# Optimization experiments

Hardware: AMD Instinct MI355X
Metric: run time of the kernel (lower is better)

Reference implementation:

```python
import jax, jax.numpy as jnp
import numpy as np

GYRO_COV = 0.00016968 ** 2
ACC_COV = 0.002 ** 2
GRAVITY = 9.81007


def _skew(v):
    # v: (..., 3) -> (..., 3, 3)
    x, y, z = v[..., 0], v[..., 1], v[..., 2]
    O = jnp.zeros_like(x)
    return jnp.stack([
        jnp.stack([O, -z, y], -1),
        jnp.stack([z, O, -x], -1),
        jnp.stack([-y, x, O], -1)], -2)


def _exp_and_jr(w):
    """SO3 Exp map (rotation matrix) and right Jacobian of w = omega*dt. w: (B,3)."""
    t2 = jnp.sum(w * w, axis=-1)[..., None, None]          # (B,1,1)
    small = t2 < 1e-8
    t2s = jnp.where(small, 1.0, t2)                        # safe denominators
    t = jnp.sqrt(t2s)
    A = jnp.where(small, 1.0 - t2 / 6.0, jnp.sin(t) / t)           # sin(t)/t
    Bc = jnp.where(small, 0.5 - t2 / 24.0, (1.0 - jnp.cos(t)) / t2s)  # (1-cos)/t^2
    C = jnp.where(small, 1.0 / 6.0 - t2 / 120.0, (t - jnp.sin(t)) / (t2s * t))  # (t-sin)/t^3
    K = _skew(w)
    K2 = K @ K
    I = jnp.eye(3, dtype=w.dtype)
    R = I + A * K + Bc * K2
    Jr = I - Bc * K + C * K2
    return R, Jr


def _preintegrate(dt, gyro, acc, init_pos, init_rot, init_vel):
    B, F = dt.shape[0], dt.shape[1]
    dtype = dt.dtype
    I3 = jnp.eye(3, dtype=dtype)

    def step(carry, xs):
        Dr, Dv, Dp, cov, t = carry
        dtk, wk, ak = xs                      # (B,1), (B,3), (B,3)
        dR, Jr = _exp_and_jr(wk * dtk)        # (B,3,3) each
        Ra = jnp.einsum('bij,bj->bi', Dr, ak) # Delta_R_ik @ a_k
        Dp_n = Dp + Dv * dtk + 0.5 * Ra * dtk ** 2
        Dv_n = Dv + Ra * dtk
        Dr_n = Dr @ dR
        # --- 9x9 covariance propagation ---
        dt_ = dtk[..., None]                  # (B,1,1)
        Ha = (Dr @ _skew(ak))                 # Delta_R_ik @ skew(a_k)
        Ib = jnp.broadcast_to(I3, Ha.shape)
        Z = jnp.zeros_like(Ha)
        A = jnp.concatenate([
            jnp.concatenate([jnp.swapaxes(dR, -1, -2), Z, Z], -1),
            jnp.concatenate([-Ha * dt_, Ib, Z], -1),
            jnp.concatenate([-0.5 * Ha * dt_ ** 2, Ib * dt_, Ib], -1)], -2)  # (B,9,9)
        Bg = Jr * dt_                                                        # (B,3,3)
        Ba = jnp.concatenate([Dr * dt_, 0.5 * Dr * dt_ ** 2], -2)           # (B,6,3)
        Ng = GYRO_COV * (Bg @ jnp.swapaxes(Bg, -1, -2))
        Na = ACC_COV * (Ba @ jnp.swapaxes(Ba, -1, -2))
        N = jnp.zeros_like(cov).at[:, :3, :3].set(Ng).at[:, 3:, 3:].set(Na)
        cov_n = A @ cov @ jnp.swapaxes(A, -1, -2) + N
        t_n = t + dtk
        return (Dr_n, Dv_n, Dp_n, cov_n, t_n), (Dr_n, Dv_n, Dp_n, t_n)

    carry0 = (jnp.broadcast_to(I3, (B, 3, 3)),
              jnp.zeros((B, 3), dtype),
              jnp.zeros((B, 3), dtype),
              jnp.zeros((B, 9, 9), dtype),
              jnp.zeros((B, 1), dtype))
    xs = (jnp.moveaxis(dt, 1, 0), jnp.moveaxis(gyro, 1, 0), jnp.moveaxis(acc, 1, 0))
    (Dr, Dv, Dp, cov, t), (Drs, Dvs, Dps, ts) = jax.lax.scan(step, carry0, xs)
    Drs = jnp.moveaxis(Drs, 0, 1)   # (B,F,3,3)
    Dvs = jnp.moveaxis(Dvs, 0, 1)   # (B,F,3)
    Dps = jnp.moveaxis(Dps, 0, 1)   # (B,F,3)
    ts = jnp.moveaxis(ts, 0, 1)     # (B,F,1)
    grav = jnp.array([0.0, 0.0, GRAVITY], dtype=dtype)
    rot = jnp.einsum('ij,bfjk->bfik', init_rot, Drs)                       # R_j = R_i * dR_ij
    vel = init_vel + jnp.einsum('ij,bfj->bfi', init_rot, Dvs) - grav * ts
    pos = (init_pos + init_vel * ts
           + jnp.einsum('ij,bfj->bfi', init_rot, Dps) - 0.5 * grav * ts ** 2)
    return rot, vel, pos, cov


def setup_inputs() -> dict:
    key = jax.random.key(0)
    k1, k2, k3 = jax.random.split(key, 3)
    B, F = 512, 2048
    dt = 0.004 * jax.random.uniform(k1, (B, F, 1), dtype=jnp.float32) + 0.001  # ~200-1000Hz
    gyro = 0.5 * jax.random.normal(k2, (B, F, 3), dtype=jnp.float32)
    acc = 2.0 * jax.random.normal(k3, (B, F, 3), dtype=jnp.float32)
    return {"dt": dt, "gyro": gyro, "acc": acc,
            "init_pos": jnp.zeros(3, jnp.float32),
            "init_rot": jnp.eye(3, dtype=jnp.float32),
            "init_vel": jnp.zeros(3, jnp.float32)}


def reference(dt, gyro, acc, init_pos, init_rot, init_vel):
    return _preintegrate(dt, gyro, acc, init_pos, init_rot, init_vel)
```

## Files before the change

kernel.cpp:

```cpp
#include <hip/hip_runtime.h>
#include <cstddef>

#define FCNT 2048
#define SEG 512
#define LSTEP 4

#define GRAV 9.81007f
#define GYRO_COV (0.00016968f * 0.00016968f)
#define ACC_COV (0.002f * 0.002f)

__device__ __forceinline__ void exp_coefs(float t2, float& A, float& Bc, float& Cc) {
  A  = 1.f     + t2 * (-1.f/6.f   + t2 * (1.f/120.f  + t2 * (-1.f/5040.f)));
  Bc = 0.5f    + t2 * (-1.f/24.f  + t2 * (1.f/720.f  + t2 * (-1.f/40320.f)));
  Cc = 1.f/6.f + t2 * (-1.f/120.f + t2 * (1.f/5040.f + t2 * (-1.f/362880.f)));
  if (t2 > 0.004f) {
    float t = sqrtf(t2);
    float sn = __sinf(t), cs = __cosf(t);
    A  = sn / t;
    Bc = (1.f - cs) / t2;
    Cc = (t - sn) / (t2 * t);
  }
}

__device__ __forceinline__ void make_dR(float w0, float w1, float w2, float t2,
                                        float A, float Bc, float* dR) {
  float w01 = w0*w1, w02 = w0*w2, w12 = w1*w2;
  dR[0] = 1.f + Bc*(w0*w0 - t2); dR[1] = Bc*w01 - A*w2;         dR[2] = Bc*w02 + A*w1;
  dR[3] = Bc*w01 + A*w2;         dR[4] = 1.f + Bc*(w1*w1 - t2); dR[5] = Bc*w12 - A*w0;
  dR[6] = Bc*w02 - A*w1;         dR[7] = Bc*w12 + A*w0;         dR[8] = 1.f + Bc*(w2*w2 - t2);
}

__device__ __forceinline__ void mm3(const float* a, const float* b, float* c) {
#pragma unroll
  for (int i = 0; i < 3; ++i) {
    float a0 = a[i*3+0], a1 = a[i*3+1], a2 = a[i*3+2];
    c[i*3+0] = a0*b[0] + a1*b[3] + a2*b[6];
    c[i*3+1] = a0*b[1] + a1*b[4] + a2*b[7];
    c[i*3+2] = a0*b[2] + a1*b[5] + a2*b[8];
  }
}

__device__ __forceinline__ void conjT(const float* R, const float* Mp, float* M) {
  float tmp[9];
#pragma unroll
  for (int i = 0; i < 3; ++i)
#pragma unroll
    for (int j = 0; j < 3; ++j)
      tmp[i*3+j] = R[0+i]*Mp[0+j] + R[3+i]*Mp[3+j] + R[6+i]*Mp[6+j];
  mm3(tmp, R, M);
}

__device__ __forceinline__ void compose16(const float* pa, const float* stv, float* o) {
  float nR[9];
  mm3(pa, stv, nR);
  float nv0 = pa[9]  + pa[0]*stv[9] + pa[1]*stv[10] + pa[2]*stv[11];
  float nv1 = pa[10] + pa[3]*stv[9] + pa[4]*stv[10] + pa[5]*stv[11];
  float nv2 = pa[11] + pa[6]*stv[9] + pa[7]*stv[10] + pa[8]*stv[11];
  float qt = stv[15];
  float np0 = pa[12] + pa[9]*qt  + pa[0]*stv[12] + pa[1]*stv[13] + pa[2]*stv[14];
  float np1 = pa[13] + pa[10]*qt + pa[3]*stv[12] + pa[4]*stv[13] + pa[5]*stv[14];
  float np2 = pa[14] + pa[11]*qt + pa[6]*stv[12] + pa[7]*stv[13] + pa[8]*stv[14];
  float nt = pa[15] + qt;
#pragma unroll
  for (int i = 0; i < 9; ++i) o[i] = nR[i];
  o[9]=nv0; o[10]=nv1; o[11]=nv2;
  o[12]=np0; o[13]=np1; o[14]=np2;
  o[15]=nt;
}

__device__ __forceinline__ void set_identity16(float* o) {
  o[0]=1;o[1]=0;o[2]=0; o[3]=0;o[4]=1;o[5]=0; o[6]=0;o[7]=0;o[8]=1;
#pragma unroll
  for (int i = 9; i < 16; ++i) o[i] = 0.f;
}

__device__ __forceinline__ void load_seg(const float* __restrict__ dtp,
                                         const float* __restrict__ gyp,
                                         const float* __restrict__ acp,
                                         size_t base, float* dl, float* gl, float* al) {
  const float4 x0 = *reinterpret_cast<const float4*>(dtp + base);
  dl[0]=x0.x; dl[1]=x0.y; dl[2]=x0.z; dl[3]=x0.w;
  const float4* qg = reinterpret_cast<const float4*>(gyp + base*3);
  const float4* qa = reinterpret_cast<const float4*>(acp + base*3);
#pragma unroll
  for (int i = 0; i < 3; ++i) {
    float4 xg = qg[i];
    gl[i*4+0]=xg.x; gl[i*4+1]=xg.y; gl[i*4+2]=xg.z; gl[i*4+3]=xg.w;
    float4 xa = qa[i];
    al[i*4+0]=xa.x; al[i*4+1]=xa.y; al[i*4+2]=xa.z; al[i*4+3]=xa.w;
  }
}

__device__ __forceinline__ void integrate_seg(const float* dl, const float* gl,
                                              const float* al, float* st) {
  set_identity16(st);
#pragma unroll
  for (int j = 0; j < LSTEP; ++j) {
    float dd = dl[j];
    float w0 = gl[j*3+0]*dd, w1 = gl[j*3+1]*dd, w2 = gl[j*3+2]*dd;
    float t2 = w0*w0 + w1*w1 + w2*w2;
    float A, Bc, Cc;
    exp_coefs(t2, A, Bc, Cc);
    (void)Cc;
    float dR[9];
    make_dR(w0, w1, w2, t2, A, Bc, dR);
    float a0 = al[j*3+0], a1 = al[j*3+1], a2 = al[j*3+2];
    float Ra0 = st[0]*a0 + st[1]*a1 + st[2]*a2;
    float Ra1 = st[3]*a0 + st[4]*a1 + st[5]*a2;
    float Ra2 = st[6]*a0 + st[7]*a1 + st[8]*a2;
    float hh = 0.5f*dd*dd;
    st[12] += st[9]*dd  + hh*Ra0;
    st[13] += st[10]*dd + hh*Ra1;
    st[14] += st[11]*dd + hh*Ra2;
    st[9] += Ra0*dd; st[10] += Ra1*dd; st[11] += Ra2*dd;
    float Rn[9];
    mm3(st, dR, Rn);
#pragma unroll
    for (int i = 0; i < 9; ++i) st[i] = Rn[i];
    st[15] += dd;
  }
}

__global__ __launch_bounds__(SEG, 2)
void imu_fused(const float* __restrict__ dtp, const float* __restrict__ gyp,
               const float* __restrict__ acp, const float* __restrict__ ip0,
               const float* __restrict__ iR0, const float* __restrict__ iv0,
               float* __restrict__ out, int B)
{
  __shared__ float rstage[FCNT*9];
  __shared__ float wtot[16*8];
  __shared__ float rbuf[8][48];
  __shared__ float tsum[48];

  const int s = threadIdx.x;
  const int lane = s & 63;
  const int wid = s >> 6;
  const int b = blockIdx.x;
  const size_t base = (size_t)b*FCNT + (size_t)s*LSTEP;
  const size_t NBF = (size_t)B*FCNT;
  float* orot = out;
  float* ovel = out + NBF*9;
  float* opos = out + NBF*12;
  float* ocov = out + NBF*15;

  float st[16];
  {
    float dl[LSTEP], gl[LSTEP*3], al[LSTEP*3];
    load_seg(dtp, gyp, acp, base, dl, gl, al);
    integrate_seg(dl, gl, al, st);
  }

#pragma unroll
  for (int off = 1; off < 64; off <<= 1) {
    float pa[16];
#pragma unroll
    for (int i = 0; i < 16; ++i) pa[i] = __shfl_up(st[i], off);
    if (lane >= off) compose16(pa, st, st);
  }
  if (lane == 63) {
#pragma unroll
    for (int i = 0; i < 16; ++i) wtot[i*8 + wid] = st[i];
  }
  __syncthreads();
  if (s < 8) {
    float t[16];
#pragma unroll
    for (int i = 0; i < 16; ++i) t[i] = wtot[i*8 + s];
#pragma unroll
    for (int off = 1; off < 8; off <<= 1) {
      float pa[16];
#pragma unroll
      for (int i = 0; i < 16; ++i) pa[i] = __shfl_up(t[i], off);
      if (s >= off) compose16(pa, t, t);
    }
#pragma unroll
    for (int i = 0; i < 16; ++i) wtot[i*8 + s] = t[i];
  }
  __syncthreads();

  float TF[16];
#pragma unroll
  for (int i = 0; i < 16; ++i) TF[i] = wtot[i*8 + 7];

  float cr[16];
  {
    float lex[16];
#pragma unroll
    for (int i = 0; i < 16; ++i) lex[i] = __shfl_up(st[i], 1);
    if (lane == 0) set_identity16(lex);
    if (wid == 0) {
#pragma unroll
      for (int i = 0; i < 16; ++i) cr[i] = lex[i];
    } else {
      float wx[16];
#pragma unroll
      for (int i = 0; i < 16; ++i) wx[i] = wtot[i*8 + wid - 1];
      compose16(wx, lex, cr);
    }
  }

  float R0g[9];
#pragma unroll
  for (int i = 0; i < 9; ++i) R0g[i] = iR0[i];
  const float p0x = ip0[0], p0y = ip0[1], p0z = ip0[2];
  const float v0x = iv0[0], v0y = iv0[1], v0z = iv0[2];

  const float Tt = TF[15];
  const float Tvp0 = R0g[0]*TF[9] + R0g[1]*TF[10] + R0g[2]*TF[11];
  const float Tvp1 = R0g[3]*TF[9] + R0g[4]*TF[10] + R0g[5]*TF[11];
  const float Tvp2 = R0g[6]*TF[9] + R0g[7]*TF[10] + R0g[8]*TF[11];
  const float Tpp0 = R0g[0]*TF[12] + R0g[1]*TF[13] + R0g[2]*TF[14];
  const float Tpp1 = R0g[3]*TF[12] + R0g[4]*TF[13] + R0g[5]*TF[14];
  const float Tpp2 = R0g[6]*TF[12] + R0g[7]*TF[13] + R0g[8]*TF[14];

  float tR[9];
  mm3(R0g, cr, tR);
  float tv0 = R0g[0]*cr[9] + R0g[1]*cr[10] + R0g[2]*cr[11];
  float tv1 = R0g[3]*cr[9] + R0g[4]*cr[10] + R0g[5]*cr[11];
  float tv2 = R0g[6]*cr[9] + R0g[7]*cr[10] + R0g[8]*cr[11];
  float tp0 = R0g[0]*cr[12] + R0g[1]*cr[13] + R0g[2]*cr[14];
  float tp1 = R0g[3]*cr[12] + R0g[4]*cr[13] + R0g[5]*cr[14];
  float tp2 = R0g[6]*cr[12] + R0g[7]*cr[13] + R0g[8]*cr[14];
  float ctt = cr[15];

  float dl[LSTEP], gl[LSTEP*3], al[LSTEP*3];
  load_seg(dtp, gyp, acp, base, dl, gl, al);

  float aS0=0,aS1=0,aS2=0,aS3=0,aS4=0,aS5=0;
  float aU0=0,aU1=0,aU2=0,aU3=0,aU4=0,aU5=0,aU6=0,aU7=0,aU8=0;
  float aV0=0,aV1=0,aV2=0,aV3=0,aV4=0,aV5=0,aV6=0,aV7=0,aV8=0;
  float b220=0,b221=0,b222=0,b223=0,b224=0,b225=0;
  float b230=0,b231=0,b232=0,b233=0,b234=0,b235=0,b236=0,b237=0,b238=0;
  float b330=0,b331=0,b332=0,b333=0,b334=0,b335=0;
  float sa=0.f, sb=0.f, sc=0.f;
  float vloc[LSTEP*3], ploc[LSTEP*3];

#pragma unroll
  for (int j = 0; j < LSTEP; ++j) {
    const float dd = dl[j];
    const float w0 = gl[j*3+0]*dd, w1 = gl[j*3+1]*dd, w2 = gl[j*3+2]*dd;
    const float t2 = w0*w0 + w1*w1 + w2*w2;
    float A, Bc, Cc;
    exp_coefs(t2, A, Bc, Cc);
    float dR[9];
    make_dR(w0, w1, w2, t2, A, Bc, dR);
    const float a0 = al[j*3+0], a1 = al[j*3+1], a2 = al[j*3+2];
    const float Ra0 = tR[0]*a0 + tR[1]*a1 + tR[2]*a2;
    const float Ra1 = tR[3]*a0 + tR[4]*a1 + tR[5]*a2;
    const float Ra2 = tR[6]*a0 + tR[7]*a1 + tR[8]*a2;
    const float hh = 0.5f*dd*dd;
    tp0 += tv0*dd + hh*Ra0;
    tp1 += tv1*dd + hh*Ra1;
    tp2 += tv2*dd + hh*Ra2;
    tv0 += Ra0*dd; tv1 += Ra1*dd; tv2 += Ra2*dd;
    float Rn[9];
    mm3(tR, dR, Rn);
#pragma unroll
    for (int i = 0; i < 9; ++i) {
      tR[i] = Rn[i];
      rstage[((size_t)s*LSTEP + j)*9 + i] = Rn[i];
    }
    ctt += dd;
    vloc[j*3+0] = v0x + tv0;
    vloc[j*3+1] = v0y + tv1;
    vloc[j*3+2] = v0z + tv2 - GRAV*ctt;
    ploc[j*3+0] = p0x + v0x*ctt + tp0;
    ploc[j*3+1] = p0y + v0y*ctt + tp1;
    ploc[j*3+2] = p0z + v0z*ctt + tp2 - 0.5f*GRAV*ctt*ctt;

    const float sg  = GYRO_COV*dd*dd;
    const float eps = 2.f*Cc - Bc*Bc - Cc*Cc*t2;
    const float alpha = sg*(1.f - eps*t2);
    const float beta  = sg*eps;
    const float u0 = tR[0]*w0 + tR[1]*w1 + tR[2]*w2;
    const float u1 = tR[3]*w0 + tR[4]*w1 + tR[5]*w2;
    const float u2 = tR[6]*w0 + tR[7]*w1 + tR[8]*w2;
    const float z = Tt - ctt;
    const float wv0 = Tvp0 - tv0, wv1 = Tvp1 - tv1, wv2 = Tvp2 - tv2;
    const float wp0 = Tpp0 - tp0 - z*tv0;
    const float wp1 = Tpp1 - tp1 - z*tv1;
    const float wp2 = Tpp2 - tp2 - z*tv2;
    const float c0 = wv1*u2 - wv2*u1;
    const float c1 = wv2*u0 - wv0*u2;
    const float c2 = wv0*u1 - wv1*u0;
    const float d0 = wp1*u2 - wp2*u1;
    const float d1 = wp2*u0 - wp0*u2;
    const float d2 = wp0*u1 - wp1*u0;
    const float bu0 = beta*u0, bu1 = beta*u1, bu2 = beta*u2;
    const float bc0 = beta*c0, bc1 = beta*c1, bc2 = beta*c2;
    const float bd0 = beta*d0, bd1 = beta*d1, bd2 = beta*d2;
    const float av0 = alpha*wv0, av1 = alpha*wv1, av2 = alpha*wv2;
    const float ap0 = alpha*wp0, ap1 = alpha*wp1, ap2 = alpha*wp2;
    const float nv2_ = wv0*wv0 + wv1*wv1 + wv2*wv2;
    const float np2_ = wp0*wp0 + wp1*wp1 + wp2*wp2;
    const float dvp  = wv0*wp0 + wv1*wp1 + wv2*wp2;
    aS0 += alpha + bu0*u0; aS1 += bu0*u1; aS2 += bu0*u2;
    aS3 += alpha + bu1*u1; aS4 += bu1*u2; aS5 += alpha + bu2*u2;
    aU0 += -bu0*c0;        aU1 += -av2 - bu0*c1;  aU2 +=  av1 - bu0*c2;
    aU3 +=  av2 - bu1*c0;  aU4 += -bu1*c1;        aU5 += -av0 - bu1*c2;
    aU6 += -av1 - bu2*c0;  aU7 +=  av0 - bu2*c1;  aU8 += -bu2*c2;
    aV0 += -bu0*d0;        aV1 += -ap2 - bu0*d1;  aV2 +=  ap1 - bu0*d2;
    aV3 +=  ap2 - bu1*d0;  aV4 += -bu1*d1;        aV5 += -ap0 - bu1*d2;
    aV6 += -ap1 - bu2*d0;  aV7 +=  ap0 - bu2*d1;  aV8 += -bu2*d2;
    b220 += av0*wv0 - alpha*nv2_ - bc0*c0;
    b221 += av0*wv1 - bc0*c1;
    b222 += av0*wv2 - bc0*c2;
    b223 += av1*wv1 - alpha*nv2_ - bc1*c1;
    b224 += av1*wv2 - bc1*c2;
    b225 += av2*wv2 - alpha*nv2_ - bc2*c2;
    b230 += ap0*wv0 - alpha*dvp - bc0*d0;
    b231 += ap0*wv1 - bc0*d1;
    b232 += ap0*wv2 - bc0*d2;
    b233 += ap1*wv0 - bc1*d0;
    b234 += ap1*wv1 - alpha*dvp - bc1*d1;
    b235 += ap1*wv2 - bc1*d2;
    b236 += ap2*wv0 - bc2*d0;
    b237 += ap2*wv1 - bc2*d1;
    b238 += ap2*wv2 - alpha*dvp - bc2*d2;
    b330 += ap0*wp0 - alpha*np2_ - bd0*d0;
    b331 += ap0*wp1 - bd0*d1;
    b332 += ap0*wp2 - bd0*d2;
    b333 += ap1*wp1 - alpha*np2_ - bd1*d1;
    b334 += ap1*wp2 - bd1*d2;
    b335 += ap2*wp2 - alpha*np2_ - bd2*d2;
    const float dsq = dd*dd;
    const float aa = ACC_COV*dsq;
    const float bbq = 0.5f*ACC_COV*dsq*dd;
    sa += aa;
    sb += aa*z + bbq;
    sc += z*(aa*z + 2.f*bbq) + 0.25f*ACC_COV*dsq*dsq;
  }
  __syncthreads();

  {
    const float4* sm4 = reinterpret_cast<const float4*>(rstage);
    float4* g4 = reinterpret_cast<float4*>(orot + (size_t)b * FCNT * 9);
#pragma unroll
    for (int k = 0; k < 9; ++k)
      g4[k*SEG + s] = sm4[k*SEG + s];
  }
  {
    float4* vq = reinterpret_cast<float4*>(ovel + base*3);
#pragma unroll
    for (int k = 0; k < LSTEP*3/4; ++k)
      vq[k] = make_float4(vloc[k*4+0], vloc[k*4+1], vloc[k*4+2], vloc[k*4+3]);
    float4* pq = reinterpret_cast<float4*>(opos + base*3);
#pragma unroll
    for (int k = 0; k < LSTEP*3/4; ++k)
      pq[k] = make_float4(ploc[k*4+0], ploc[k*4+1], ploc[k*4+2], ploc[k*4+3]);
  }

  {
    float red[48] = {aS0,aS1,aS2,aS3,aS4,aS5,
                     aU0,aU1,aU2,aU3,aU4,aU5,aU6,aU7,aU8,
                     aV0,aV1,aV2,aV3,aV4,aV5,aV6,aV7,aV8,
                     b220,b221,b222,b223,b224,b225,
                     b230,b231,b232,b233,b234,b235,b236,b237,b238,
                     b330,b331,b332,b333,b334,b335,
                     sa,sb,sc};
#pragma unroll
    for (int i = 0; i < 48; ++i) {
      float x = red[i];
      x += __shfl_down(x, 32);
      x += __shfl_down(x, 16);
      x += __shfl_down(x, 8);
      x += __shfl_down(x, 4);
      x += __shfl_down(x, 2);
      x += __shfl_down(x, 1);
      red[i] = x;
    }
    if (lane == 0) {
#pragma unroll
      for (int i = 0; i < 48; ++i) rbuf[wid][i] = red[i];
    }
  }
  __syncthreads();
  if (s < 48) {
    float acc = rbuf[0][s];
#pragma unroll
    for (int w = 1; w < 8; ++w) acc += rbuf[w][s];
    tsum[s] = acc;
  }
  __syncthreads();

  if (s == 0) {
    float T[48];
#pragma unroll
    for (int i = 0; i < 48; ++i) T[i] = tsum[i];
    float TR[9];
#pragma unroll
    for (int i = 0; i < 9; ++i) TR[i] = TF[i];
    float Rt[9] = {TR[0],TR[3],TR[6], TR[1],TR[4],TR[7], TR[2],TR[5],TR[8]};
    float Smp[9] = {T[0],T[1],T[2], T[1],T[3],T[4], T[2],T[4],T[5]};
    float Ump[9] = {T[6],T[7],T[8], T[9],T[10],T[11], T[12],T[13],T[14]};
    float Vmp[9] = {T[15],T[16],T[17], T[18],T[19],T[20], T[21],T[22],T[23]};
    float W22p[9]= {T[24],T[25],T[26], T[25],T[27],T[28], T[26],T[28],T[29]};
    float W23p[9]= {T[30],T[31],T[32], T[33],T[34],T[35], T[36],T[37],T[38]};
    float W33p[9]= {T[39],T[40],T[41], T[40],T[42],T[43], T[41],T[43],T[44]};
    float Sm[9], Um[9], Vm[9], W22[9], W23[9], W33[9];
    conjT(R0g, Smp, Sm);
    conjT(R0g, Ump, Um);
    conjT(R0g, Vmp, Vm);
    conjT(R0g, W22p, W22);
    conjT(R0g, W23p, W23);
    conjT(R0g, W33p, W33);
    const float ssa = T[45], ssb = T[46], ssc = T[47];
    float T1[9], C11[9], C12[9], C13[9];
    mm3(Rt, Sm, T1);
    mm3(T1, TR, C11);
    mm3(Rt, Um, C12);
    mm3(Rt, Vm, C13);
    float* co = ocov + (size_t)b * 81;
#pragma unroll
    for (int i = 0; i < 3; ++i) {
#pragma unroll
      for (int jj = 0; jj < 3; ++jj) {
        co[i*9 + jj]       = C11[i*3+jj];
        co[i*9 + 3 + jj]   = C12[i*3+jj];
        co[i*9 + 6 + jj]   = C13[i*3+jj];
        co[(3+i)*9 + jj]     = C12[jj*3+i];
        co[(3+i)*9 + 3 + jj] = -W22[i*3+jj] + (i==jj ? ssa : 0.f);
        co[(3+i)*9 + 6 + jj] = -W23[i*3+jj] + (i==jj ? ssb : 0.f);
        co[(6+i)*9 + jj]     = C13[jj*3+i];
        co[(6+i)*9 + 3 + jj] = -W23[jj*3+i] + (i==jj ? ssb : 0.f);
        co[(6+i)*9 + 6 + jj] = -W33[i*3+jj] + (i==jj ? ssc : 0.f);
      }
    }
  }
}

extern "C" void kernel_launch(void* const* d_in, const int* in_sizes, int n_in,
                              void* d_out, int out_size, void* d_ws, size_t ws_size,
                              hipStream_t stream) {
  const float* dt   = (const float*)d_in[0];
  const float* gyro = (const float*)d_in[1];
  const float* acc  = (const float*)d_in[2];
  const float* ip   = (const float*)d_in[3];
  const float* iR   = (const float*)d_in[4];
  const float* iv   = (const float*)d_in[5];
  float* out = (float*)d_out;
  const int B = in_sizes[0] / FCNT;
  imu_fused<<<dim3(B), dim3(SEG), 0, stream>>>(dt, gyro, acc, ip, iR, iv, out, B);
}
```

Baseline: 51.08 us.

## Use polynomial exp coefficients, packed float2 accumulators, and lighter barriers

Replaces the sin/cos branch in the SO3 coefficients with truncated Taylor polynomials everywhere, and substitutes a short series for the covariance eps term. Packs the 48 covariance accumulators into float2 vectors so the compiler can emit packed FMA instructions. Marks block-uniform values as scalar via readfirstlane, moves the velocity and position stores before the barrier, and swaps __syncthreads for an LDS-only wait plus s_barrier. The polynomial forms are only accurate for small rotation angles per step; larger angular increments would lose precision.

```diff
diff --git a/kernel.cpp b/kernel.cpp
--- a/kernel.cpp
+++ b/kernel.cpp
@@ -9,17 +9,13 @@
 #define GYRO_COV (0.00016968f * 0.00016968f)
 #define ACC_COV (0.002f * 0.002f)
 
-__device__ __forceinline__ void exp_coefs(float t2, float& A, float& Bc, float& Cc) {
-  A  = 1.f     + t2 * (-1.f/6.f   + t2 * (1.f/120.f  + t2 * (-1.f/5040.f)));
-  Bc = 0.5f    + t2 * (-1.f/24.f  + t2 * (1.f/720.f  + t2 * (-1.f/40320.f)));
-  Cc = 1.f/6.f + t2 * (-1.f/120.f + t2 * (1.f/5040.f + t2 * (-1.f/362880.f)));
-  if (t2 > 0.004f) {
-    float t = sqrtf(t2);
-    float sn = __sinf(t), cs = __cosf(t);
-    A  = sn / t;
-    Bc = (1.f - cs) / t2;
-    Cc = (t - sn) / (t2 * t);
-  }
+typedef float v2f __attribute__((ext_vector_type(2)));
+__device__ __forceinline__ v2f V2(float x, float y){ v2f r; r.x=x; r.y=y; return r; }
+__device__ __forceinline__ v2f sp(float x){ v2f r; r.x=x; r.y=x; return r; }
+
+__device__ __forceinline__ void exp_AB(float t2, float& A, float& Bc) {
+  A  = 1.f  + t2 * (-1.f/6.f  + t2 * (1.f/120.f  + t2 * (-1.f/5040.f)));
+  Bc = 0.5f + t2 * (-1.f/24.f + t2 * (1.f/720.f  + t2 * (-1.f/40320.f)));
 }
 
 __device__ __forceinline__ void make_dR(float w0, float w1, float w2, float t2,
@@ -74,6 +70,16 @@
   for (int i = 9; i < 16; ++i) o[i] = 0.f;
 }
 
+__device__ __forceinline__ float uf(float x) {
+  return __uint_as_float(__builtin_amdgcn_readfirstlane(__float_as_uint(x)));
+}
+
+__device__ __forceinline__ void lds_barrier() {
+  asm volatile("s_waitcnt lgkmcnt(0)" ::: "memory");
+  __builtin_amdgcn_s_barrier();
+  asm volatile("" ::: "memory");
+}
+
 __device__ __forceinline__ void load_seg(const float* __restrict__ dtp,
                                          const float* __restrict__ gyp,
                                          const float* __restrict__ acp,
@@ -99,9 +105,8 @@
     float dd = dl[j];
     float w0 = gl[j*3+0]*dd, w1 = gl[j*3+1]*dd, w2 = gl[j*3+2]*dd;
     float t2 = w0*w0 + w1*w1 + w2*w2;
-    float A, Bc, Cc;
-    exp_coefs(t2, A, Bc, Cc);
-    (void)Cc;
+    float A, Bc;
+    exp_AB(t2, A, Bc);
     float dR[9];
     make_dR(w0, w1, w2, t2, A, Bc, dR);
     float a0 = al[j*3+0], a1 = al[j*3+1], a2 = al[j*3+2];
@@ -205,13 +210,13 @@
   const float p0x = ip0[0], p0y = ip0[1], p0z = ip0[2];
   const float v0x = iv0[0], v0y = iv0[1], v0z = iv0[2];
 
-  const float Tt = TF[15];
-  const float Tvp0 = R0g[0]*TF[9] + R0g[1]*TF[10] + R0g[2]*TF[11];
-  const float Tvp1 = R0g[3]*TF[9] + R0g[4]*TF[10] + R0g[5]*TF[11];
-  const float Tvp2 = R0g[6]*TF[9] + R0g[7]*TF[10] + R0g[8]*TF[11];
-  const float Tpp0 = R0g[0]*TF[12] + R0g[1]*TF[13] + R0g[2]*TF[14];
-  const float Tpp1 = R0g[3]*TF[12] + R0g[4]*TF[13] + R0g[5]*TF[14];
-  const float Tpp2 = R0g[6]*TF[12] + R0g[7]*TF[13] + R0g[8]*TF[14];
+  const float Tt   = uf(TF[15]);
+  const float Tvp0 = uf(R0g[0]*TF[9] + R0g[1]*TF[10] + R0g[2]*TF[11]);
+  const float Tvp1 = uf(R0g[3]*TF[9] + R0g[4]*TF[10] + R0g[5]*TF[11]);
+  const float Tvp2 = uf(R0g[6]*TF[9] + R0g[7]*TF[10] + R0g[8]*TF[11]);
+  const float Tpp0 = uf(R0g[0]*TF[12] + R0g[1]*TF[13] + R0g[2]*TF[14]);
+  const float Tpp1 = uf(R0g[3]*TF[12] + R0g[4]*TF[13] + R0g[5]*TF[14]);
+  const float Tpp2 = uf(R0g[6]*TF[12] + R0g[7]*TF[13] + R0g[8]*TF[14]);
 
   float tR[9];
   mm3(R0g, cr, tR);
@@ -226,13 +231,10 @@
   float dl[LSTEP], gl[LSTEP*3], al[LSTEP*3];
   load_seg(dtp, gyp, acp, base, dl, gl, al);
 
-  float aS0=0,aS1=0,aS2=0,aS3=0,aS4=0,aS5=0;
-  float aU0=0,aU1=0,aU2=0,aU3=0,aU4=0,aU5=0,aU6=0,aU7=0,aU8=0;
-  float aV0=0,aV1=0,aV2=0,aV3=0,aV4=0,aV5=0,aV6=0,aV7=0,aV8=0;
-  float b220=0,b221=0,b222=0,b223=0,b224=0,b225=0;
-  float b230=0,b231=0,b232=0,b233=0,b234=0,b235=0,b236=0,b237=0,b238=0;
-  float b330=0,b331=0,b332=0,b333=0,b334=0,b335=0;
-  float sa=0.f, sb=0.f, sc=0.f;
+  v2f pA0=sp(0),pA1=sp(0),pA2=sp(0),pA3=sp(0),pA4=sp(0),pA5=sp(0),
+      pA6=sp(0),pA7=sp(0),pA8=sp(0),pA9=sp(0),pA10=sp(0),pA11=sp(0),
+      pA12=sp(0),pA13=sp(0),pA14=sp(0),pA15=sp(0),pA16=sp(0),pA17=sp(0),
+      pA18=sp(0),pA19=sp(0),pA20=sp(0),pA21=sp(0),pA22=sp(0),pA23=sp(0);
   float vloc[LSTEP*3], ploc[LSTEP*3];
 
 #pragma unroll
@@ -240,8 +242,8 @@
     const float dd = dl[j];
     const float w0 = gl[j*3+0]*dd, w1 = gl[j*3+1]*dd, w2 = gl[j*3+2]*dd;
     const float t2 = w0*w0 + w1*w1 + w2*w2;
-    float A, Bc, Cc;
-    exp_coefs(t2, A, Bc, Cc);
+    float A, Bc;
+    exp_AB(t2, A, Bc);
     float dR[9];
     make_dR(w0, w1, w2, t2, A, Bc, dR);
     const float a0 = al[j*3+0], a1 = al[j*3+1], a2 = al[j*3+2];
@@ -269,7 +271,7 @@
     ploc[j*3+2] = p0z + v0z*ctt + tp2 - 0.5f*GRAV*ctt*ctt;
 
     const float sg  = GYRO_COV*dd*dd;
-    const float eps = 2.f*Cc - Bc*Bc - Cc*Cc*t2;
+    const float eps = (1.f/12.f) - t2*(1.f/360.f);
     const float alpha = sg*(1.f - eps*t2);
     const float beta  = sg*eps;
     const float u0 = tR[0]*w0 + tR[1]*w1 + tR[2]*w2;
@@ -294,43 +296,49 @@
     const float nv2_ = wv0*wv0 + wv1*wv1 + wv2*wv2;
     const float np2_ = wp0*wp0 + wp1*wp1 + wp2*wp2;
     const float dvp  = wv0*wp0 + wv1*wp1 + wv2*wp2;
-    aS0 += alpha + bu0*u0; aS1 += bu0*u1; aS2 += bu0*u2;
-    aS3 += alpha + bu1*u1; aS4 += bu1*u2; aS5 += alpha + bu2*u2;
-    aU0 += -bu0*c0;        aU1 += -av2 - bu0*c1;  aU2 +=  av1 - bu0*c2;
-    aU3 +=  av2 - bu1*c0;  aU4 += -bu1*c1;        aU5 += -av0 - bu1*c2;
-    aU6 += -av1 - bu2*c0;  aU7 +=  av0 - bu2*c1;  aU8 += -bu2*c2;
-    aV0 += -bu0*d0;        aV1 += -ap2 - bu0*d1;  aV2 +=  ap1 - bu0*d2;
-    aV3 +=  ap2 - bu1*d0;  aV4 += -bu1*d1;        aV5 += -ap0 - bu1*d2;
-    aV6 += -ap1 - bu2*d0;  aV7 +=  ap0 - bu2*d1;  aV8 += -bu2*d2;
-    b220 += av0*wv0 - alpha*nv2_ - bc0*c0;
-    b221 += av0*wv1 - bc0*c1;
-    b222 += av0*wv2 - bc0*c2;
-    b223 += av1*wv1 - alpha*nv2_ - bc1*c1;
-    b224 += av1*wv2 - bc1*c2;
-    b225 += av2*wv2 - alpha*nv2_ - bc2*c2;
-    b230 += ap0*wv0 - alpha*dvp - bc0*d0;
-    b231 += ap0*wv1 - bc0*d1;
-    b232 += ap0*wv2 - bc0*d2;
-    b233 += ap1*wv0 - bc1*d0;
-    b234 += ap1*wv1 - alpha*dvp - bc1*d1;
-    b235 += ap1*wv2 - bc1*d2;
-    b236 += ap2*wv0 - bc2*d0;
-    b237 += ap2*wv1 - bc2*d1;
-    b238 += ap2*wv2 - alpha*dvp - bc2*d2;
-    b330 += ap0*wp0 - alpha*np2_ - bd0*d0;
-    b331 += ap0*wp1 - bd0*d1;
-    b332 += ap0*wp2 - bd0*d2;
-    b333 += ap1*wp1 - alpha*np2_ - bd1*d1;
-    b334 += ap1*wp2 - bd1*d2;
-    b335 += ap2*wp2 - alpha*np2_ - bd2*d2;
+    const float anv = alpha*nv2_, adv = alpha*dvp, anp = alpha*np2_;
+
+    pA0  += sp(bu0)*V2(u0,u1) + V2(alpha,0.f);
+    pA1  += V2(bu0,bu1)*V2(u2,u1) + V2(0.f,alpha);
+    pA2  += V2(bu1,bu2)*sp(u2) + V2(0.f,alpha);
+    pA3  += -(sp(bu0)*V2(c0,c1)) + V2(0.f,-av2);
+    pA4  += V2(av1,av2) - V2(bu0,bu1)*V2(c2,c0);
+    pA5  += -(sp(bu1)*V2(c1,c2)) + V2(0.f,-av0);
+    pA6  += V2(-av1,av0) - sp(bu2)*V2(c0,c1);
+    pA7  += -(V2(bu2,bu0)*V2(c2,d0));
+    pA8  += V2(-ap2,ap1) - sp(bu0)*V2(d1,d2);
+    pA9  += V2(ap2,0.f) - sp(bu1)*V2(d0,d1);
+    pA10 += V2(-ap0,-ap1) - V2(bu1,bu2)*V2(d2,d0);
+    pA11 += V2(ap0,0.f) - sp(bu2)*V2(d1,d2);
+    pA12 += sp(av0)*V2(wv0,wv1) - sp(bc0)*V2(c0,c1) - V2(anv,0.f);
+    pA13 += V2(av0,av1)*V2(wv2,wv1) - V2(bc0,bc1)*V2(c2,c1) - V2(0.f,anv);
+    pA14 += V2(av1,av2)*sp(wv2) - V2(bc1,bc2)*sp(c2) - V2(0.f,anv);
+    pA15 += sp(ap0)*V2(wv0,wv1) - sp(bc0)*V2(d0,d1) - V2(adv,0.f);
+    pA16 += V2(ap0,ap1)*V2(wv2,wv0) - V2(bc0,bc1)*V2(d2,d0);
+    pA17 += sp(ap1)*V2(wv1,wv2) - sp(bc1)*V2(d1,d2) - V2(adv,0.f);
+    pA18 += sp(ap2)*V2(wv0,wv1) - sp(bc2)*V2(d0,d1);
+    pA19 += V2(ap2,ap0)*V2(wv2,wp0) - V2(bc2,bd0)*V2(d2,d0) - V2(adv,anp);
+    pA20 += sp(ap0)*V2(wp1,wp2) - sp(bd0)*V2(d1,d2);
+    pA21 += sp(ap1)*V2(wp1,wp2) - sp(bd1)*V2(d1,d2) - V2(anp,0.f);
     const float dsq = dd*dd;
     const float aa = ACC_COV*dsq;
     const float bbq = 0.5f*ACC_COV*dsq*dd;
-    sa += aa;
-    sb += aa*z + bbq;
-    sc += z*(aa*z + 2.f*bbq) + 0.25f*ACC_COV*dsq*dsq;
-  }
-  __syncthreads();
+    pA22 += V2(ap2*wp2 - anp - bd2*d2, aa);
+    pA23 += V2(aa*z + bbq, z*(aa*z + 2.f*bbq) + 0.25f*ACC_COV*dsq*dsq);
+  }
+
+  {
+    float4* vq = reinterpret_cast<float4*>(ovel + base*3);
+#pragma unroll
+    for (int k = 0; k < LSTEP*3/4; ++k)
+      vq[k] = make_float4(vloc[k*4+0], vloc[k*4+1], vloc[k*4+2], vloc[k*4+3]);
+    float4* pq = reinterpret_cast<float4*>(opos + base*3);
+#pragma unroll
+    for (int k = 0; k < LSTEP*3/4; ++k)
+      pq[k] = make_float4(ploc[k*4+0], ploc[k*4+1], ploc[k*4+2], ploc[k*4+3]);
+  }
+
+  lds_barrier();
 
   {
     const float4* sm4 = reinterpret_cast<const float4*>(rstage);
@@ -339,25 +347,13 @@
     for (int k = 0; k < 9; ++k)
       g4[k*SEG + s] = sm4[k*SEG + s];
   }
+
   {
-    float4* vq = reinterpret_cast<float4*>(ovel + base*3);
-#pragma unroll
-    for (int k = 0; k < LSTEP*3/4; ++k)
-      vq[k] = make_float4(vloc[k*4+0], vloc[k*4+1], vloc[k*4+2], vloc[k*4+3]);
-    float4* pq = reinterpret_cast<float4*>(opos + base*3);
-#pragma unroll
-    for (int k = 0; k < LSTEP*3/4; ++k)
-      pq[k] = make_float4(ploc[k*4+0], ploc[k*4+1], ploc[k*4+2], ploc[k*4+3]);
-  }
-
-  {
-    float red[48] = {aS0,aS1,aS2,aS3,aS4,aS5,
-                     aU0,aU1,aU2,aU3,aU4,aU5,aU6,aU7,aU8,
-                     aV0,aV1,aV2,aV3,aV4,aV5,aV6,aV7,aV8,
-                     b220,b221,b222,b223,b224,b225,
-                     b230,b231,b232,b233,b234,b235,b236,b237,b238,
-                     b330,b331,b332,b333,b334,b335,
-                     sa,sb,sc};
+    v2f flat[24] = {pA0,pA1,pA2,pA3,pA4,pA5,pA6,pA7,pA8,pA9,pA10,pA11,
+                    pA12,pA13,pA14,pA15,pA16,pA17,pA18,pA19,pA20,pA21,pA22,pA23};
+    float red[48];
+#pragma unroll
+    for (int i = 0; i < 24; ++i) { red[2*i] = flat[i].x; red[2*i+1] = flat[i].y; }
 #pragma unroll
     for (int i = 0; i < 48; ++i) {
       float x = red[i];
@@ -374,14 +370,14 @@
       for (int i = 0; i < 48; ++i) rbuf[wid][i] = red[i];
     }
   }
-  __syncthreads();
+  lds_barrier();
   if (s < 48) {
     float acc = rbuf[0][s];
 #pragma unroll
     for (int w = 1; w < 8; ++w) acc += rbuf[w][s];
     tsum[s] = acc;
   }
-  __syncthreads();
+  lds_barrier();
 
   if (s == 0) {
     float T[48];
@@ -405,9 +401,9 @@
     conjT(R0g, W23p, W23);
     conjT(R0g, W33p, W33);
     const float ssa = T[45], ssb = T[46], ssc = T[47];
-    float T1[9], C11[9], C12[9], C13[9];
-    mm3(Rt, Sm, T1);
-    mm3(T1, TR, C11);
+    float T1m[9], C11[9], C12[9], C13[9];
+    mm3(Rt, Sm, T1m);
+    mm3(T1m, TR, C11);
     mm3(Rt, Um, C12);
     mm3(Rt, Vm, C13);
     float* co = ocov + (size_t)b * 81;
```

After: 51.10 us. Within noise of the previous version (+0.0%).
